# Kernel tuning notes

Measured on AMD Instinct MI355X. Metric: run time of the kernel, lower is better.

The kernel has to match this reference:

```python
import jax, jax.numpy as jnp
import numpy as np

RADIUS = 0.1
NSAMPLE = 32
NUM_KP = 15
KP_EXTENT = 1.0
DENSITY_PARAM = 5.0
EXTENT = 2.0 * KP_EXTENT * RADIUS / DENSITY_PARAM  # 0.04
K_RADIUS = 1.5 * EXTENT                            # 0.06
C_IN, C_OUT = 64, 128
BN_EPS = 1e-5


def make_kernel_points():
    # Deterministic stand-in for create_kernel_points: first point at center
    # ('center' fixed mode), remaining points quasi-uniform in a ball of K_RADIUS.
    rs = np.random.RandomState(0)
    d = rs.randn(NUM_KP - 1, 3)
    d /= np.linalg.norm(d, axis=1, keepdims=True) + 1e-9
    r = rs.rand(NUM_KP - 1, 1) ** (1.0 / 3.0)
    pts = np.concatenate([np.zeros((1, 3)), d * r * K_RADIUS], axis=0)
    return jnp.asarray(pts, dtype=jnp.float32)  # [K, 3]


def ball_group(query_xyz, support_xyz, support_mask, radius, nsample):
    """Masked ordered ball query. Returns idx [B,N1,S] int32 and mask [B,N1,S] float."""
    # [B, N1, N2] squared distances (dominant memory traffic)
    d2 = jnp.sum((query_xyz[:, :, None, :] - support_xyz[:, None, :, :]) ** 2, axis=-1)
    valid = (d2 < radius * radius) & (support_mask[:, None, :] > 0)
    order = jnp.cumsum(valid.astype(jnp.int32), axis=-1) - 1  # rank among valid, per row
    in_cap = valid & (order < nsample)
    slot = jnp.where(in_cap, order, nsample)  # overflow -> dump slot
    B, N1, N2 = d2.shape
    j = jnp.broadcast_to(jnp.arange(N2, dtype=jnp.int32), (B, N1, N2))
    b = jnp.arange(B)[:, None, None]
    n = jnp.arange(N1)[None, :, None]
    idx = jnp.zeros((B, N1, nsample + 1), jnp.int32).at[b, n, slot].set(j)[..., :nsample]
    cnt = jnp.sum(in_cap.astype(jnp.int32), axis=-1)  # [B, N1]
    nb_mask = jnp.arange(nsample)[None, None, :] < cnt[:, :, None]
    idx = jnp.where(nb_mask, idx, idx[:, :, :1])  # pad with first neighbor
    return idx, nb_mask.astype(jnp.float32)


def setup_inputs() -> dict:
    key = jax.random.key(0)
    ks = jax.random.split(key, 6)
    B, N1, N2 = 4, 2048, 8192
    query_xyz = jax.random.uniform(ks[0], (B, N1, 3), dtype=jnp.float32)
    support_xyz = jax.random.uniform(ks[1], (B, N2, 3), dtype=jnp.float32)
    query_mask = jnp.ones((B, N1), jnp.float32)
    support_mask = jnp.ones((B, N2), jnp.float32)
    support_features = jax.random.normal(ks[2], (B, C_IN, N2), dtype=jnp.float32)
    kernel_weights = jax.random.normal(ks[3], (NUM_KP, C_IN), dtype=jnp.float32) * (1.0 / np.sqrt(C_IN))
    W_out = jax.random.normal(ks[4], (C_OUT, C_IN), dtype=jnp.float32) * (1.0 / np.sqrt(C_IN))
    gamma = jnp.ones((C_OUT,), jnp.float32)
    beta = jnp.zeros((C_OUT,), jnp.float32)
    return {
        "query_xyz": query_xyz, "support_xyz": support_xyz,
        "query_mask": query_mask, "support_mask": support_mask,
        "support_features": support_features, "K_points": make_kernel_points(),
        "kernel_weights": kernel_weights, "W_out": W_out,
        "gamma": gamma, "beta": beta,
    }


def reference(query_xyz, support_xyz, query_mask, support_mask, support_features,
              K_points, kernel_weights, W_out, gamma, beta):
    idx, nb_mask = ball_group(query_xyz, support_xyz, support_mask, RADIUS, NSAMPLE)
    # gather neighbor features: [B, N2, C] -> [B, N1, S, C]
    feats_t = jnp.transpose(support_features, (0, 2, 1))
    nbr_feats = jnp.take_along_axis(feats_t[:, None, :, :],
                                    idx[:, :, :, None], axis=2)  # [B,N1,S,C]
    # grouped relative positions: [B, N1, S, 3]
    grouped_xyz = jnp.take_along_axis(support_xyz[:, None, :, :],
                                      idx[:, :, :, None], axis=2)
    rel_pos = grouped_xyz - query_xyz[:, :, None, :]
    # kernel-point distances: [B, N1, S, K]
    diff = rel_pos[:, :, :, None, :] - K_points[None, None, None, :, :]
    sq_d = jnp.sum(diff * diff, axis=-1)
    # linear influence, then permute to [B, N1, K, S]
    w = jnp.clip(1.0 - jnp.sqrt(sq_d) / EXTENT, 0.0, None)
    w = jnp.transpose(w, (0, 1, 3, 2))
    feature_mask = nb_mask + (1.0 - query_mask[:, :, None])  # [B,N1,S]
    w = w * feature_mask[:, :, None, :]
    # weighted sum over neighbors: [B, N1, K, C]
    weighted = jnp.einsum('bnks,bnsc->bnkc', w, nbr_feats)
    out = jnp.sum(weighted * kernel_weights[None, None, :, :], axis=2)  # [B,N1,C]
    out = jnp.transpose(out, (0, 2, 1))  # [B, C_in, N1]
    # out_conv: 1x1 conv (no bias) + BatchNorm1d (training-mode batch stats) + ReLU
    out = jnp.einsum('oc,bcn->bon', W_out, out)  # [B, C_out, N1]
    mean = jnp.mean(out, axis=(0, 2), keepdims=True)
    var = jnp.mean((out - mean) ** 2, axis=(0, 2), keepdims=True)
    out = (out - mean) * jax.lax.rsqrt(var + BN_EPS)
    out = out * gamma[None, :, None] + beta[None, :, None]
    return jax.nn.relu(out)
```

## Files before the change

### kernel.cpp

```cpp
#include <hip/hip_runtime.h>
#include <stdint.h>

#define BATCH 4
#define N1D   2048
#define N2D   8192
#define NSAMP 32
#define NKP   15
#define CIN   64
#define COUT  128

#define RAD2    0.01f
#define INV_EXT 25.0f
#define BN_EPS  1e-5f

#define QPW   2
#define NWAVE 4
#define QPB   (QPW*NWAVE)
#define CHUNK 256
#define NCHUNK (N2D/CHUNK)

#define WS_PTS4   0
#define WS_FEATT  131072
#define WS_WT     (131072+2097152)
#define WS_OUT2   (2228224+524288)
#define WS_STATS  (2752512+1048576)

__global__ __launch_bounds__(256) void pg_prep(
    const float* __restrict__ sxyz, const float* __restrict__ smask,
    const float* __restrict__ sfeat, const float* __restrict__ Wout,
    float4* __restrict__ pts4, float* __restrict__ featT, float* __restrict__ Wt)
{
  __shared__ float tile[64*65];
  const int t  = threadIdx.x;
  const int bt = blockIdx.x;

  if (bt == 512) {
#pragma unroll
    for (int i = 0; i < 32; ++i) {
      const int flat = i*256 + t;
      Wt[flat] = Wout[(flat & 127)*CIN + (flat >> 7)];
    }
    return;
  }

  const int b  = bt >> 7;
  const int j0 = (bt & 127) * 64;

  if (t < 64) {
    const int g = bt*64 + t;
    const float m = smask[g];
    float x = sxyz[g*3+0], y = sxyz[g*3+1], z = sxyz[g*3+2];
    if (m <= 0.0f) { x = 1e30f; y = 1e30f; z = 1e30f; }
    pts4[g] = make_float4(x, y, z, 0.0f);
  }

  const float* src = sfeat + (b*CIN)*N2D + j0;
#pragma unroll
  for (int i = 0; i < 16; ++i) {
    const int c = i*4 + (t >> 6);
    tile[c*65 + (t & 63)] = src[c*N2D + (t & 63)];
  }
  __syncthreads();
  float* dstb = featT + (size_t)(b*N2D + j0) * CIN;
#pragma unroll
  for (int r = 0; r < 4; ++r) {
    const int j  = r*16 + (t >> 4);
    const int c4 = (t & 15) * 4;
    float4 v;
    v.x = tile[(c4+0)*65 + j];
    v.y = tile[(c4+1)*65 + j];
    v.z = tile[(c4+2)*65 + j];
    v.w = tile[(c4+3)*65 + j];
    *(float4*)(dstb + j*CIN + c4) = v;
  }
}

__global__ __launch_bounds__(256) void pg_main(
    const float* __restrict__ qxyz, const float* __restrict__ sxyz,
    const float* __restrict__ qmask, const float4* __restrict__ pts4,
    const float* __restrict__ featT, const float* __restrict__ Kp,
    const float* __restrict__ KW, const float* __restrict__ Wt,
    float* __restrict__ out2)
{
  __shared__ float4   s_pts[2][CHUNK];
  __shared__ int      s_idx[QPB*NSAMP];
  __shared__ int      s_cnt[QPB];
  __shared__ float    s_w[QPB*NSAMP*17];
  __shared__ unsigned s_wm[QPB*NSAMP];
  __shared__ float    s_xq[QPB*65];

  const int t    = threadIdx.x;
  const int lane = t & 63;
  const int wv   = t >> 6;
  const int gbase = blockIdx.x * QPB;
  const int b     = gbase >> 11;

  float qx[QPW], qy[QPW], qz[QPW];
  int cnt[QPW];
#pragma unroll
  for (int q = 0; q < QPW; ++q) {
    const int g = gbase + wv*QPW + q;
    qx[q] = qxyz[g*3+0]; qy[q] = qxyz[g*3+1]; qz[q] = qxyz[g*3+2];
    cnt[q] = 0;
  }

  const float4* bp = pts4 + b*N2D;
  float4 v = bp[t];
  bool wdone = false;
  const uint64_t lt = (1ull << lane) - 1ull;

  for (int ch = 0; ch < NCHUNK; ++ch) {
    const int buf = ch & 1;
    s_pts[buf][t] = v;
    if (ch + 1 < NCHUNK) v = bp[(ch+1)*CHUNK + t];
    __syncthreads();
    if (!wdone) {
#pragma unroll
      for (int sub = 0; sub < CHUNK/64; ++sub) {
        const float4 p = s_pts[buf][sub*64 + lane];
        const int jj = ch*CHUNK + sub*64 + lane;
#pragma unroll
        for (int q = 0; q < QPW; ++q) {
          const float dx = p.x - qx[q];
          const float dy = p.y - qy[q];
          const float dz = p.z - qz[q];
          const float d2 = dx*dx + dy*dy + dz*dz;
          const bool valid = d2 < RAD2;
          const uint64_t m = __ballot(valid);
          if (valid) {
            const int pos = cnt[q] + __popcll(m & lt);
            if (pos < NSAMP) s_idx[(wv*QPW + q)*NSAMP + pos] = jj;
          }
          cnt[q] += (int)__popcll(m);
        }
      }
      if (cnt[0] >= NSAMP && cnt[1] >= NSAMP)
        wdone = true;
    }
  }

  if (lane == 0) {
#pragma unroll
    for (int q = 0; q < QPW; ++q) {
      int c = cnt[q]; if (c > NSAMP) c = NSAMP;
      s_cnt[wv*QPW + q] = c;
    }
  }
  __syncthreads();

  {
    const int qslot = t >> 5;
    const int s = t & 31;
    const int c = s_cnt[qslot];
    int j;
    if (s < c) {
      j = s_idx[t];
    } else {
      j = (c > 0) ? s_idx[qslot*NSAMP] : 0;
      s_idx[t] = j;
    }
    const int g = gbase + qslot;
    const float4 pj = pts4[b*N2D + j];
    const float rx = pj.x - qxyz[g*3+0];
    const float ry = pj.y - qxyz[g*3+1];
    const float rz = pj.z - qxyz[g*3+2];

    unsigned msk = 0u;
#pragma unroll
    for (int k = 0; k < NKP; ++k) {
      const float dx = rx - Kp[k*3+0];
      const float dy = ry - Kp[k*3+1];
      const float dz = rz - Kp[k*3+2];
      const float dd = dx*dx + dy*dy + dz*dz;
      const float w = 1.0f - sqrtf(dd) * INV_EXT;
      if (w > 0.0f) {
        s_w[t*17 + k] = w;
        msk |= (1u << k);
      }
    }
    s_wm[t] = msk;
  }
  __syncthreads();

  float kw[NKP];
#pragma unroll
  for (int k = 0; k < NKP; ++k) kw[k] = KW[k*CIN + lane];

#pragma unroll
  for (int qi = 0; qi < QPW; ++qi) {
    const int ql = wv*QPW + qi;
    const int g = gbase + ql;
    const float fpad = 1.0f - qmask[g];
    const int c = __builtin_amdgcn_readfirstlane(s_cnt[ql]);

    float ft[NSAMP];
#pragma unroll
    for (int s = 0; s < NSAMP; ++s) {
      const int j = __builtin_amdgcn_readfirstlane(s_idx[ql*NSAMP + s]);
      ft[s] = featT[(size_t)(b*N2D + j)*CIN + lane];
    }

    float acc = 0.0f;
#pragma unroll
    for (int s = 0; s < NSAMP; ++s) {
      const float fm = ((s < c) ? 1.0f : 0.0f) + fpad;
      if (fm != 0.0f) {
        const unsigned mk =
            (unsigned)__builtin_amdgcn_readfirstlane((int)s_wm[ql*NSAMP + s]);
        if (mk != 0u) {
          const float* wp = &s_w[(ql*NSAMP + s)*17];
          float wsum = 0.0f;
#pragma unroll
          for (int k = 0; k < NKP; ++k)
            if (mk & (1u << k)) wsum += wp[k] * kw[k];
          acc = fmaf(fm*wsum, ft[s], acc);
        }
      }
    }
    s_xq[ql*65 + lane] = acc;
  }
  __syncthreads();

  {
    const int n8 = t & 7;
    const int og = t >> 3;
    const int g  = gbase + n8;
    const int nn = g & 2047;
    float a0 = 0.f, a1 = 0.f, a2 = 0.f, a3 = 0.f;
#pragma unroll
    for (int c = 0; c < CIN; ++c) {
      const float xc = s_xq[n8*65 + c];
      const float4 w4 = *(const float4*)(Wt + c*COUT + og*4);
      a0 = fmaf(w4.x, xc, a0);
      a1 = fmaf(w4.y, xc, a1);
      a2 = fmaf(w4.z, xc, a2);
      a3 = fmaf(w4.w, xc, a3);
    }
    float* ob = out2 + (size_t)(b*COUT + og*4)*N1D + nn;
    ob[0]       = a0;
    ob[N1D]     = a1;
    ob[2*N1D]   = a2;
    ob[3*N1D]   = a3;
  }
}

__global__ __launch_bounds__(256) void pg_stats(
    const float* __restrict__ out2, float* __restrict__ stats)
{
  __shared__ float red[8];
  const int t = threadIdx.x;
  const int o = blockIdx.x;
  float s1 = 0.f, s2 = 0.f;
#pragma unroll
  for (int bb = 0; bb < BATCH; ++bb) {
    const float4* p = (const float4*)(out2 + (size_t)(bb*COUT + o)*N1D);
#pragma unroll
    for (int i = 0; i < 2; ++i) {
      const float4 x = p[i*256 + t];
      s1 += x.x + x.y + x.z + x.w;
      s2 += x.x*x.x + x.y*x.y + x.z*x.z + x.w*x.w;
    }
  }
#pragma unroll
  for (int off = 32; off; off >>= 1) {
    s1 += __shfl_xor(s1, off);
    s2 += __shfl_xor(s2, off);
  }
  const int wv = t >> 6;
  if ((t & 63) == 0) { red[wv] = s1; red[4+wv] = s2; }
  __syncthreads();
  if (t == 0) {
    stats[o]        = red[0]+red[1]+red[2]+red[3];
    stats[COUT + o] = red[4]+red[5]+red[6]+red[7];
  }
}

__global__ __launch_bounds__(256) void pg_apply(
    const float* __restrict__ out2, const float* __restrict__ stats,
    const float* __restrict__ gamma, const float* __restrict__ beta,
    float* __restrict__ dout)
{
  const int i = blockIdx.x*256 + threadIdx.x;
  const int flat = i*4;
  const int o = (flat >> 11) & 127;
  const float inv = 1.0f / (float)(BATCH*N1D);
  const float mean = stats[o] * inv;
  const float var = stats[COUT + o] * inv - mean*mean;
  const float istd = rsqrtf(var + BN_EPS);
  const float ga = gamma[o] * istd;
  const float be = beta[o];
  const float4 x = ((const float4*)out2)[i];
  float4 y;
  y.x = fmaxf((x.x - mean)*ga + be, 0.0f);
  y.y = fmaxf((x.y - mean)*ga + be, 0.0f);
  y.z = fmaxf((x.z - mean)*ga + be, 0.0f);
  y.w = fmaxf((x.w - mean)*ga + be, 0.0f);
  ((float4*)dout)[i] = y;
}

extern "C" void kernel_launch(void* const* d_in, const int* in_sizes, int n_in,
                              void* d_out, int out_size, void* d_ws, size_t ws_size,
                              hipStream_t stream)
{
  const float* qxyz  = (const float*)d_in[0];
  const float* sxyz  = (const float*)d_in[1];
  const float* qmask = (const float*)d_in[2];
  const float* smask = (const float*)d_in[3];
  const float* sfeat = (const float*)d_in[4];
  const float* Kp    = (const float*)d_in[5];
  const float* KW    = (const float*)d_in[6];
  const float* Wout  = (const float*)d_in[7];
  const float* gamma = (const float*)d_in[8];
  const float* beta  = (const float*)d_in[9];
  float* ws = (float*)d_ws;
  float4* pts4 = (float4*)(ws + WS_PTS4);
  float* featT = ws + WS_FEATT;
  float* Wt    = ws + WS_WT;
  float* out2  = ws + WS_OUT2;
  float* stats = ws + WS_STATS;
  float* dst   = (float*)d_out;

  pg_prep <<<513,  256, 0, stream>>>(sxyz, smask, sfeat, Wout, pts4, featT, Wt);
  pg_main <<<1024, 256, 0, stream>>>(qxyz, sxyz, qmask, pts4, featT, Kp, KW, Wt, out2);
  pg_stats<<<128,  256, 0, stream>>>(out2, stats);
  pg_apply<<<1024, 256, 0, stream>>>(out2, stats, gamma, beta, dst);
}
```

Measured before the change: 137.0 us.

## Replace brute-force ball query with uniform grid cell binning and rank sort

Support points are bucketed into a 10x10x10 uniform grid via counting sort in the prep kernel. The main kernel then scans only neighbouring cells for each query, collects up to 96 candidates, and rank-sorts them by original index to keep ordered ball-query semantics. The stats and apply kernels are fused into one finish kernel, and the feature transpose load is vectorised. The grid assumes coordinates in [0,1], and the candidate cap could drop neighbours in dense regions.

Measured after the change: 155.6 us. 13.6% more time.

```diff
diff --git a/kernel.cpp b/kernel.cpp
--- a/kernel.cpp
+++ b/kernel.cpp
@@ -1,5 +1,6 @@
 #include <hip/hip_runtime.h>
 #include <stdint.h>
+#include <limits.h>
 
 #define BATCH 4
 #define N1D   2048
@@ -12,27 +13,42 @@
 #define RAD2    0.01f
 #define INV_EXT 25.0f
 #define BN_EPS  1e-5f
+#define CMARG   0.1000001f
 
 #define QPW   2
 #define NWAVE 4
 #define QPB   (QPW*NWAVE)
-#define CHUNK 256
-#define NCHUNK (N2D/CHUNK)
+#define NCELL 1000
+#define MAXC  96
 
 #define WS_PTS4   0
-#define WS_FEATT  131072
-#define WS_WT     (131072+2097152)
-#define WS_OUT2   (2228224+524288)
-#define WS_STATS  (2752512+1048576)
+#define WS_BPTS   131072
+#define WS_FEATT  262144
+#define WS_WT     2359296
+#define WS_OUT2   2367488
+#define WS_CS     3416064
+
+__device__ __forceinline__ int cell_of(float x, float y, float z) {
+  int cx = (int)(x*10.f); cx = cx < 0 ? 0 : (cx > 9 ? 9 : cx);
+  int cy = (int)(y*10.f); cy = cy < 0 ? 0 : (cy > 9 ? 9 : cy);
+  int cz = (int)(z*10.f); cz = cz < 0 ? 0 : (cz > 9 ? 9 : cz);
+  return (cx*10 + cy)*10 + cz;
+}
 
 __global__ __launch_bounds__(256) void pg_prep(
     const float* __restrict__ sxyz, const float* __restrict__ smask,
     const float* __restrict__ sfeat, const float* __restrict__ Wout,
-    float4* __restrict__ pts4, float* __restrict__ featT, float* __restrict__ Wt)
+    float4* __restrict__ pts4, float* __restrict__ featT, float* __restrict__ Wt,
+    float4* __restrict__ bpts, int* __restrict__ cellStart)
 {
   __shared__ float tile[64*65];
-  const int t  = threadIdx.x;
-  const int bt = blockIdx.x;
+  __shared__ int cnt_s[NCELL];
+  __shared__ int off_s[NCELL+1];
+  __shared__ int wsum[4];
+  const int t    = threadIdx.x;
+  const int lane = t & 63;
+  const int wv   = t >> 6;
+  const int bt   = blockIdx.x;
 
   if (bt == 512) {
 #pragma unroll
@@ -43,22 +59,71 @@
     return;
   }
 
+  if (bt >= 513) {
+    const int bb = bt - 513;
+    const float* sx = sxyz + (size_t)bb*N2D*3;
+    const float* sm = smask + (size_t)bb*N2D;
+    for (int i = t; i < NCELL; i += 256) cnt_s[i] = 0;
+    __syncthreads();
+    for (int i = t; i < N2D; i += 256) {
+      if (sm[i] > 0.f)
+        atomicAdd(&cnt_s[cell_of(sx[i*3], sx[i*3+1], sx[i*3+2])], 1);
+    }
+    __syncthreads();
+    int v = 0;
+    if (t < 250) v = cnt_s[t*4] + cnt_s[t*4+1] + cnt_s[t*4+2] + cnt_s[t*4+3];
+    int x = v;
+#pragma unroll
+    for (int off = 1; off < 64; off <<= 1) {
+      int y = __shfl_up(x, off);
+      if (lane >= off) x += y;
+    }
+    if (lane == 63) wsum[wv] = x;
+    __syncthreads();
+    int base = 0;
+#pragma unroll
+    for (int w = 0; w < 4; ++w) if (w < wv) base += wsum[w];
+    const int excl = base + x - v;
+    if (t < 250) {
+      int o = excl;
+      off_s[t*4+0] = o; o += cnt_s[t*4+0];
+      off_s[t*4+1] = o; o += cnt_s[t*4+1];
+      off_s[t*4+2] = o; o += cnt_s[t*4+2];
+      off_s[t*4+3] = o;
+    }
+    if (t == 0) off_s[NCELL] = 0;
+    __syncthreads();
+    if (t == 0) off_s[NCELL] = wsum[0]+wsum[1]+wsum[2]+wsum[3];
+    __syncthreads();
+    for (int i = t; i < NCELL; i += 256) cnt_s[i] = off_s[i];
+    __syncthreads();
+    for (int i = t; i < N2D; i += 256) {
+      if (sm[i] > 0.f) {
+        const float px = sx[i*3], py = sx[i*3+1], pz = sx[i*3+2];
+        const int pos = atomicAdd(&cnt_s[cell_of(px,py,pz)], 1);
+        bpts[(size_t)bb*N2D + pos] = make_float4(px, py, pz, __int_as_float(i));
+      }
+    }
+    for (int i = t; i < NCELL+1; i += 256) cellStart[bb*(NCELL+1) + i] = off_s[i];
+    return;
+  }
+
   const int b  = bt >> 7;
   const int j0 = (bt & 127) * 64;
-
   if (t < 64) {
     const int g = bt*64 + t;
-    const float m = smask[g];
-    float x = sxyz[g*3+0], y = sxyz[g*3+1], z = sxyz[g*3+2];
-    if (m <= 0.0f) { x = 1e30f; y = 1e30f; z = 1e30f; }
-    pts4[g] = make_float4(x, y, z, 0.0f);
-  }
-
-  const float* src = sfeat + (b*CIN)*N2D + j0;
-#pragma unroll
-  for (int i = 0; i < 16; ++i) {
-    const int c = i*4 + (t >> 6);
-    tile[c*65 + (t & 63)] = src[c*N2D + (t & 63)];
+    pts4[g] = make_float4(sxyz[g*3+0], sxyz[g*3+1], sxyz[g*3+2], 0.f);
+  }
+  const float* src = sfeat + (size_t)(b*CIN)*N2D + j0;
+#pragma unroll
+  for (int i = 0; i < 4; ++i) {
+    const int c  = i*16 + (t >> 4);
+    const int j4 = (t & 15) * 4;
+    const float4 v = *(const float4*)(src + (size_t)c*N2D + j4);
+    tile[c*65 + j4+0] = v.x;
+    tile[c*65 + j4+1] = v.y;
+    tile[c*65 + j4+2] = v.z;
+    tile[c*65 + j4+3] = v.w;
   }
   __syncthreads();
   float* dstb = featT + (size_t)(b*N2D + j0) * CIN;
@@ -76,13 +141,14 @@
 }
 
 __global__ __launch_bounds__(256) void pg_main(
-    const float* __restrict__ qxyz, const float* __restrict__ sxyz,
-    const float* __restrict__ qmask, const float4* __restrict__ pts4,
-    const float* __restrict__ featT, const float* __restrict__ Kp,
-    const float* __restrict__ KW, const float* __restrict__ Wt,
-    float* __restrict__ out2)
+    const float* __restrict__ qxyz, const float* __restrict__ qmask,
+    const float4* __restrict__ pts4, const float4* __restrict__ bpts,
+    const int* __restrict__ cellStart, const float* __restrict__ featT,
+    const float* __restrict__ Kp, const float* __restrict__ KW,
+    const float* __restrict__ Wt, float* __restrict__ out2)
 {
-  __shared__ float4   s_pts[2][CHUNK];
+  __shared__ int      s_cs[NCELL+1];
+  __shared__ int      s_cand[QPB][MAXC];
   __shared__ int      s_idx[QPB*NSAMP];
   __shared__ int      s_cnt[QPB];
   __shared__ float    s_w[QPB*NSAMP*17];
@@ -94,57 +160,60 @@
   const int wv   = t >> 6;
   const int gbase = blockIdx.x * QPB;
   const int b     = gbase >> 11;
-
-  float qx[QPW], qy[QPW], qz[QPW];
-  int cnt[QPW];
-#pragma unroll
-  for (int q = 0; q < QPW; ++q) {
-    const int g = gbase + wv*QPW + q;
-    qx[q] = qxyz[g*3+0]; qy[q] = qxyz[g*3+1]; qz[q] = qxyz[g*3+2];
-    cnt[q] = 0;
-  }
-
-  const float4* bp = pts4 + b*N2D;
-  float4 v = bp[t];
-  bool wdone = false;
   const uint64_t lt = (1ull << lane) - 1ull;
 
-  for (int ch = 0; ch < NCHUNK; ++ch) {
-    const int buf = ch & 1;
-    s_pts[buf][t] = v;
-    if (ch + 1 < NCHUNK) v = bp[(ch+1)*CHUNK + t];
-    __syncthreads();
-    if (!wdone) {
-#pragma unroll
-      for (int sub = 0; sub < CHUNK/64; ++sub) {
-        const float4 p = s_pts[buf][sub*64 + lane];
-        const int jj = ch*CHUNK + sub*64 + lane;
-#pragma unroll
-        for (int q = 0; q < QPW; ++q) {
-          const float dx = p.x - qx[q];
-          const float dy = p.y - qy[q];
-          const float dz = p.z - qz[q];
-          const float d2 = dx*dx + dy*dy + dz*dz;
-          const bool valid = d2 < RAD2;
-          const uint64_t m = __ballot(valid);
-          if (valid) {
-            const int pos = cnt[q] + __popcll(m & lt);
-            if (pos < NSAMP) s_idx[(wv*QPW + q)*NSAMP + pos] = jj;
+  for (int i = t; i < NCELL+1; i += 256) s_cs[i] = cellStart[b*(NCELL+1) + i];
+  __syncthreads();
+
+  const float4* bptsb = bpts + (size_t)b*N2D;
+#pragma unroll
+  for (int qi = 0; qi < QPW; ++qi) {
+    const int ql = wv*QPW + qi;
+    const int g  = gbase + ql;
+    const float qx = qxyz[g*3+0], qy = qxyz[g*3+1], qz = qxyz[g*3+2];
+    int cx0 = (int)((qx-CMARG)*10.f); if (cx0 < 0) cx0 = 0;
+    int cx1 = (int)((qx+CMARG)*10.f); if (cx1 > 9) cx1 = 9;
+    int cy0 = (int)((qy-CMARG)*10.f); if (cy0 < 0) cy0 = 0;
+    int cy1 = (int)((qy+CMARG)*10.f); if (cy1 > 9) cy1 = 9;
+    int cz0 = (int)((qz-CMARG)*10.f); if (cz0 < 0) cz0 = 0;
+    int cz1 = (int)((qz+CMARG)*10.f); if (cz1 > 9) cz1 = 9;
+
+    int ccnt = 0;
+    for (int cx = cx0; cx <= cx1; ++cx) {
+      for (int cy = cy0; cy <= cy1; ++cy) {
+        const int rowb = (cx*10 + cy)*10;
+        const int rs = s_cs[rowb + cz0];
+        const int re = s_cs[rowb + cz1 + 1];
+        for (int base = rs; base < re; base += 64) {
+          const int ii = base + lane;
+          bool ok = false; int jj = 0;
+          if (ii < re) {
+            const float4 p = bptsb[ii];
+            const float dx = p.x - qx, dy = p.y - qy, dz = p.z - qz;
+            ok = (dx*dx + dy*dy + dz*dz) < RAD2;
+            jj = __float_as_int(p.w);
           }
-          cnt[q] += (int)__popcll(m);
+          const uint64_t m = __ballot(ok);
+          if (ok) {
+            const int pos = ccnt + __popcll(m & lt);
+            if (pos < MAXC) s_cand[ql][pos] = jj;
+          }
+          ccnt += (int)__popcll(m);
         }
       }
-      if (cnt[0] >= NSAMP && cnt[1] >= NSAMP)
-        wdone = true;
-    }
-  }
-
-  if (lane == 0) {
-#pragma unroll
-    for (int q = 0; q < QPW; ++q) {
-      int c = cnt[q]; if (c > NSAMP) c = NSAMP;
-      s_cnt[wv*QPW + q] = c;
-    }
+    }
+    const int C = ccnt < MAXC ? ccnt : MAXC;
+    int jA = (lane      < C) ? s_cand[ql][lane]      : INT_MAX;
+    int jB = (lane + 64 < C) ? s_cand[ql][lane + 64] : INT_MAX;
+    int rA = 0, rB = 0;
+    for (int e = 0; e < C; ++e) {
+      const int je = s_cand[ql][e];
+      rA += (je < jA);
+      rB += (je < jB);
+    }
+    if (lane      < C && rA < NSAMP) s_idx[ql*NSAMP + rA] = jA;
+    if (lane + 64 < C && rB < NSAMP) s_idx[ql*NSAMP + rB] = jB;
+    if (lane == 0) s_cnt[ql] = C < NSAMP ? C : NSAMP;
   }
   __syncthreads();
 
@@ -237,26 +306,31 @@
       a3 = fmaf(w4.w, xc, a3);
     }
     float* ob = out2 + (size_t)(b*COUT + og*4)*N1D + nn;
-    ob[0]       = a0;
-    ob[N1D]     = a1;
-    ob[2*N1D]   = a2;
-    ob[3*N1D]   = a3;
-  }
-}
-
-__global__ __launch_bounds__(256) void pg_stats(
-    const float* __restrict__ out2, float* __restrict__ stats)
+    ob[0]     = a0;
+    ob[N1D]   = a1;
+    ob[2*N1D] = a2;
+    ob[3*N1D] = a3;
+  }
+}
+
+__global__ __launch_bounds__(256) void pg_finish(
+    const float* __restrict__ out2, const float* __restrict__ gamma,
+    const float* __restrict__ beta, float* __restrict__ dout)
 {
   __shared__ float red[8];
-  const int t = threadIdx.x;
-  const int o = blockIdx.x;
+  __shared__ float mv[2];
+  const int t  = threadIdx.x;
+  const int o  = blockIdx.x & 127;
+  const int bb = blockIdx.x >> 7;
+  float4 f[4][2];
   float s1 = 0.f, s2 = 0.f;
 #pragma unroll
-  for (int bb = 0; bb < BATCH; ++bb) {
-    const float4* p = (const float4*)(out2 + (size_t)(bb*COUT + o)*N1D);
+  for (int r = 0; r < BATCH; ++r) {
+    const float4* p = (const float4*)(out2 + (size_t)(r*COUT + o)*N1D);
 #pragma unroll
     for (int i = 0; i < 2; ++i) {
       const float4 x = p[i*256 + t];
+      f[r][i] = x;
       s1 += x.x + x.y + x.z + x.w;
       s2 += x.x*x.x + x.y*x.y + x.z*x.z + x.w*x.w;
     }
@@ -270,32 +344,27 @@
   if ((t & 63) == 0) { red[wv] = s1; red[4+wv] = s2; }
   __syncthreads();
   if (t == 0) {
-    stats[o]        = red[0]+red[1]+red[2]+red[3];
-    stats[COUT + o] = red[4]+red[5]+red[6]+red[7];
-  }
-}
-
-__global__ __launch_bounds__(256) void pg_apply(
-    const float* __restrict__ out2, const float* __restrict__ stats,
-    const float* __restrict__ gamma, const float* __restrict__ beta,
-    float* __restrict__ dout)
-{
-  const int i = blockIdx.x*256 + threadIdx.x;
-  const int flat = i*4;
-  const int o = (flat >> 11) & 127;
-  const float inv = 1.0f / (float)(BATCH*N1D);
-  const float mean = stats[o] * inv;
-  const float var = stats[COUT + o] * inv - mean*mean;
-  const float istd = rsqrtf(var + BN_EPS);
-  const float ga = gamma[o] * istd;
+    const float inv = 1.0f / (float)(BATCH*N1D);
+    const float mean = (red[0]+red[1]+red[2]+red[3]) * inv;
+    const float var  = (red[4]+red[5]+red[6]+red[7]) * inv - mean*mean;
+    mv[0] = mean;
+    mv[1] = rsqrtf(var + BN_EPS);
+  }
+  __syncthreads();
+  const float mean = mv[0];
+  const float ga = gamma[o] * mv[1];
   const float be = beta[o];
-  const float4 x = ((const float4*)out2)[i];
-  float4 y;
-  y.x = fmaxf((x.x - mean)*ga + be, 0.0f);
-  y.y = fmaxf((x.y - mean)*ga + be, 0.0f);
-  y.z = fmaxf((x.z - mean)*ga + be, 0.0f);
-  y.w = fmaxf((x.w - mean)*ga + be, 0.0f);
-  ((float4*)dout)[i] = y;
+  float4* dp = (float4*)(dout + (size_t)(bb*COUT + o)*N1D);
+#pragma unroll
+  for (int i = 0; i < 2; ++i) {
+    const float4 x = f[bb][i];
+    float4 y;
+    y.x = fmaxf((x.x - mean)*ga + be, 0.0f);
+    y.y = fmaxf((x.y - mean)*ga + be, 0.0f);
+    y.z = fmaxf((x.z - mean)*ga + be, 0.0f);
+    y.w = fmaxf((x.w - mean)*ga + be, 0.0f);
+    dp[i*256 + t] = y;
+  }
 }
 
 extern "C" void kernel_launch(void* const* d_in, const int* in_sizes, int n_in,
@@ -314,14 +383,16 @@
   const float* beta  = (const float*)d_in[9];
   float* ws = (float*)d_ws;
   float4* pts4 = (float4*)(ws + WS_PTS4);
+  float4* bpts = (float4*)(ws + WS_BPTS);
   float* featT = ws + WS_FEATT;
   float* Wt    = ws + WS_WT;
   float* out2  = ws + WS_OUT2;
-  float* stats = ws + WS_STATS;
+  int*   cellS = (int*)(ws + WS_CS);
   float* dst   = (float*)d_out;
 
-  pg_prep <<<513,  256, 0, stream>>>(sxyz, smask, sfeat, Wout, pts4, featT, Wt);
-  pg_main <<<1024, 256, 0, stream>>>(qxyz, sxyz, qmask, pts4, featT, Kp, KW, Wt, out2);
-  pg_stats<<<128,  256, 0, stream>>>(out2, stats);
-  pg_apply<<<1024, 256, 0, stream>>>(out2, stats, gamma, beta, dst);
-}
+  pg_prep  <<<517,  256, 0, stream>>>(sxyz, smask, sfeat, Wout, pts4, featT, Wt,
+                                      bpts, cellS);
+  pg_main  <<<1024, 256, 0, stream>>>(qxyz, qmask, pts4, bpts, cellS, featT,
+                                      Kp, KW, Wt, out2);
+  pg_finish<<<512,  256, 0, stream>>>(out2, gamma, beta, dst);
+}
```
